# Kernel optimization log

Hardware: AMD Instinct MI355X
Metric: run time of the kernel (lower is better)

## Reference

```python
import jax, jax.numpy as jnp
import numpy as np
import math

CHUNK = 256
NUM_HEADS = 4
EPS = 1e-5


def setup_inputs() -> dict:
    key = jax.random.key(0)
    ks = jax.random.split(key, 12)
    B, N, F = 4, 2048, 256
    x = jax.random.normal(ks[0], (B, N, F), dtype=jnp.float32)
    adj_matrix = jax.random.randint(ks[1], (N, N), 0, 2, dtype=jnp.int32)
    s = 1.0 / math.sqrt(F)
    Wq = jax.random.normal(ks[2], (F, F), dtype=jnp.float32) * s
    bq = jnp.zeros((F,), dtype=jnp.float32)
    Wk = jax.random.normal(ks[3], (F, F), dtype=jnp.float32) * s
    bk = jnp.zeros((F,), dtype=jnp.float32)
    Wv = jax.random.normal(ks[4], (F, F), dtype=jnp.float32) * s
    bv = jnp.zeros((F,), dtype=jnp.float32)
    Wo = jax.random.normal(ks[5], (F, F), dtype=jnp.float32) * s
    bo = jnp.zeros((F,), dtype=jnp.float32)
    gamma = jnp.ones((F,), dtype=jnp.float32)
    beta = jnp.zeros((F,), dtype=jnp.float32)
    return {"x": x, "adj_matrix": adj_matrix, "Wq": Wq, "bq": bq, "Wk": Wk,
            "bk": bk, "Wv": Wv, "bv": bv, "Wo": Wo, "bo": bo,
            "gamma": gamma, "beta": beta}


def reference(x, adj_matrix, Wq, bq, Wk, bk, Wv, bv, Wo, bo, gamma, beta):
    B, N, Fin = x.shape
    H = NUM_HEADS
    Dout = Wq.shape[0]
    Dh = Dout // H
    Nc = N // CHUNK  # number of key chunks

    # projections -> [B, H, N, Dh]
    q = (x @ Wq.T + bq).reshape(B, N, H, Dh).transpose(0, 2, 1, 3)
    k = (x @ Wk.T + bk).reshape(B, N, H, Dh).transpose(0, 2, 1, 3)
    v = (x @ Wv.T + bv).reshape(B, N, H, Dh).transpose(0, 2, 1, 3)

    # key/value chunks: [B, H, Nc, CHUNK, Dh]
    kc = k.reshape(B, H, Nc, CHUNK, Dh)
    vc = v.reshape(B, H, Nc, CHUNK, Dh)

    # scores per key chunk: [B, H, N, Nc, CHUNK]
    scores = jnp.einsum('bhnd,bhjcd->bhnjc', q, kc) / jnp.sqrt(
        jnp.asarray(Dh, dtype=q.dtype))
    scores = jnp.clip(scores, -10.0, 10.0)
    # adjacency mask, chunked along keys: [1, 1, N, Nc, CHUNK]
    mask = adj_matrix.reshape(N, Nc, CHUNK)[None, None]
    scores = jnp.where(mask == 0, jnp.asarray(-10.0, scores.dtype), scores)

    # FAITHFUL quirk: softmax is taken per key chunk (last axis only) and the
    # per-chunk contexts are SUMMED -> total attention mass per query is Nc.
    attn = jax.nn.softmax(scores, axis=-1)
    ctx = jnp.einsum('bhnjc,bhjcd->bhnd', attn, vc)  # sum over chunks j

    ctx = ctx.transpose(0, 2, 1, 3).reshape(B, N, Dout)
    out = ctx @ Wo.T + bo
    out = out + x  # residual (in_features == out_features)

    mu = jnp.mean(out, axis=-1, keepdims=True)
    var = jnp.mean(jnp.square(out - mu), axis=-1, keepdims=True)
    out = (out - mu) * jax.lax.rsqrt(var + EPS) * gamma + beta
    return out
```

## Files before the change

kernel.cpp:

```cpp
#include <hip/hip_runtime.h>
#include <math.h>

#define B_     4
#define N_     2048
#define F_     256
#define H_     4
#define DH     64
#define BN     8192
#define SP     72
#define SPW    264

#define QSCALE 0.18033688011112042f
#define CLIP   14.426950408889634f

typedef _Float16 f16;
typedef _Float16 half8  __attribute__((ext_vector_type(8)));
typedef _Float16 half4v __attribute__((ext_vector_type(4)));
typedef float    floatx4 __attribute__((ext_vector_type(4)));
typedef unsigned long long u64;

__device__ __forceinline__ half8 cvt8(float4 a, float4 b) {
    half8 h;
    h[0] = (f16)a.x; h[1] = (f16)a.y; h[2] = (f16)a.z; h[3] = (f16)a.w;
    h[4] = (f16)b.x; h[5] = (f16)b.y; h[6] = (f16)b.z; h[7] = (f16)b.w;
    return h;
}

__global__ __launch_bounds__(256) void pack_adj(
    const int* __restrict__ adj, u64* __restrict__ P)
{
    const int row   = blockIdx.x >> 3;
    const int chunk = blockIdx.x & 7;
    const int wave  = threadIdx.x >> 6, lane = threadIdx.x & 63;
    const int key   = chunk * 256 + wave * 64 + lane;
    u64 m = __ballot(adj[(size_t)row * N_ + key] != 0);
    if (lane == 0) P[(size_t)row * 32 + chunk * 4 + wave] = m;
}

__global__ __launch_bounds__(256) void cvt_wo(
    const float* __restrict__ Wo, f16* __restrict__ Woh)
{
    const int idx = (blockIdx.x * 256 + threadIdx.x) * 4;
    float4 v = *(const float4*)(Wo + idx);
    half4v h; h[0] = (f16)v.x; h[1] = (f16)v.y; h[2] = (f16)v.z; h[3] = (f16)v.w;
    *(half4v*)(Woh + idx) = h;
}

__global__ __launch_bounds__(256) void proj_mfma(
    const float* __restrict__ x,
    const float* __restrict__ Wq, const float* __restrict__ Wk, const float* __restrict__ Wv,
    const float* __restrict__ bq, const float* __restrict__ bk, const float* __restrict__ bv,
    f16* __restrict__ Qh, f16* __restrict__ Kh, f16* __restrict__ Vt)
{
    const int which = blockIdx.z;
    const float* W    = which == 0 ? Wq : which == 1 ? Wk : Wv;
    const float* bias = which == 0 ? bq : which == 1 ? bk : bv;

    const int r0 = blockIdx.x * 64;
    const int hy = blockIdx.y;
    const int c0 = hy * 64;
    const int tid  = threadIdx.x;
    const int wave = tid >> 6, lane = tid & 63;
    const int quad = lane >> 4, l16 = lane & 15;
    const int row = tid >> 2, seg = tid & 3;

    __shared__ f16 xs[64 * SP];
    __shared__ f16 wsm[64 * SP];

    floatx4 zz = {0.f, 0.f, 0.f, 0.f};
    floatx4 acc[4] = {zz, zz, zz, zz};

    for (int f0 = 0; f0 < F_; f0 += 64) {
        const float* xsrc = x + (size_t)(r0 + row) * F_ + f0 + seg * 16;
        const float* wsrc = W + (size_t)(c0 + row) * F_ + f0 + seg * 16;
        float4 xa0 = *(const float4*)(xsrc + 0), xa1 = *(const float4*)(xsrc + 4);
        float4 xa2 = *(const float4*)(xsrc + 8), xa3 = *(const float4*)(xsrc + 12);
        float4 wa0 = *(const float4*)(wsrc + 0), wa1 = *(const float4*)(wsrc + 4);
        float4 wa2 = *(const float4*)(wsrc + 8), wa3 = *(const float4*)(wsrc + 12);
        __syncthreads();
        *(half8*)&xs[row * SP + seg * 16]      = cvt8(xa0, xa1);
        *(half8*)&xs[row * SP + seg * 16 + 8]  = cvt8(xa2, xa3);
        *(half8*)&wsm[row * SP + seg * 16]     = cvt8(wa0, wa1);
        *(half8*)&wsm[row * SP + seg * 16 + 8] = cvt8(wa2, wa3);
        __syncthreads();
#pragma unroll
        for (int s = 0; s < 2; s++) {
            half8 af = *(const half8*)&xs[(wave * 16 + l16) * SP + s * 32 + quad * 8];
#pragma unroll
            for (int ot = 0; ot < 4; ot++) {
                half8 bf = *(const half8*)&wsm[(ot * 16 + l16) * SP + s * 32 + quad * 8];
                acc[ot] = __builtin_amdgcn_mfma_f32_16x16x32_f16(af, bf, acc[ot], 0, 0, 0);
            }
        }
    }

    const int bb = r0 >> 11, nn0 = r0 & (N_ - 1);

    if (which == 2) {
#pragma unroll
        for (int ot = 0; ot < 4; ot++) {
            const float bv_ = bias[c0 + ot * 16 + l16];
            half4v h4;
#pragma unroll
            for (int r = 0; r < 4; r++) h4[r] = (f16)(acc[ot][r] + bv_);
            *(half4v*)(Vt + (((size_t)bb * H_ + hy) * DH + ot * 16 + l16) * N_
                          + nn0 + wave * 16 + quad * 4) = h4;
        }
    } else {
        const float scl = (which == 0) ? QSCALE : 1.0f;
        f16* dst = which == 0 ? Qh : Kh;
        __syncthreads();
        f16* outb = xs;
#pragma unroll
        for (int ot = 0; ot < 4; ot++) {
            const float bv_ = bias[c0 + ot * 16 + l16];
#pragma unroll
            for (int r = 0; r < 4; r++)
                outb[(wave * 16 + quad * 4 + r) * SP + ot * 16 + l16] =
                    (f16)((acc[ot][r] + bv_) * scl);
        }
        __syncthreads();
        f16* g = dst + (((size_t)bb * H_ + hy) * N_ + nn0 + row) * DH + seg * 16;
        *(float4*)(g)     = *(const float4*)&outb[row * SP + seg * 16];
        *(float4*)(g + 8) = *(const float4*)&outb[row * SP + seg * 16 + 8];
    }
}

__global__ __launch_bounds__(256) void attn_mfma(
    const f16* __restrict__ Qh, const f16* __restrict__ Kh,
    const f16* __restrict__ Vt, const u64* __restrict__ Padj,
    f16* __restrict__ CTXP)
{
    const int nt = blockIdx.x & 31;
    const int sp = blockIdx.x >> 5;
    const int qb = nt * 64;
    const int h  = blockIdx.y;
    const int b  = blockIdx.z;
    const int bh = b * H_ + h;
    const int tid  = threadIdx.x;
    const int wave = tid >> 6, lane = tid & 63;
    const int quad = lane >> 4, l16 = lane & 15;
    const int row = tid >> 2, seg = tid & 3;

    __shared__ f16 QPs[64 * SP];
    __shared__ f16 Ks[64 * SP];
    __shared__ f16 Vs[64 * SP];

    {
        const f16* src = Qh + ((size_t)bh * N_ + qb + row) * DH + seg * 16;
        *(float4*)&QPs[row * SP + seg * 16]     = *(const float4*)(src);
        *(float4*)&QPs[row * SP + seg * 16 + 8] = *(const float4*)(src + 8);
    }
    __syncthreads();
    const half8 qf0 = *(const half8*)&QPs[(wave * 16 + l16) * SP + quad * 8];
    const half8 qf1 = *(const half8*)&QPs[(wave * 16 + l16) * SP + 32 + quad * 8];
    f16* Ps = QPs + wave * 16 * SP;

    const int qglob = qb + wave * 16 + l16;
    const u64* arow = Padj + (size_t)qglob * 32;

    floatx4 zz = {0.f, 0.f, 0.f, 0.f};
    floatx4 ctx_tot[4] = {zz, zz, zz, zz};

    for (int ci = 0; ci < 2; ci++) {
        const int c = sp * 2 + ci;
        floatx4 ctx_ch[4] = {zz, zz, zz, zz};
        float rs_ch = 0.f;

        for (int kt = 0; kt < 4; kt++) {
            const int k0 = c * 256 + kt * 64;
            const f16* ksrc = Kh + ((size_t)bh * N_ + k0 + row) * DH + seg * 16;
            const f16* vsrc = Vt + ((size_t)bh * DH + row) * N_ + k0 + seg * 16;
            float4 ka0 = *(const float4*)(ksrc), ka1 = *(const float4*)(ksrc + 8);
            float4 va0 = *(const float4*)(vsrc), va1 = *(const float4*)(vsrc + 8);
            __syncthreads();
            *(float4*)&Ks[row * SP + seg * 16]     = ka0;
            *(float4*)&Ks[row * SP + seg * 16 + 8] = ka1;
            *(float4*)&Vs[row * SP + seg * 16]     = va0;
            *(float4*)&Vs[row * SP + seg * 16 + 8] = va1;
            __syncthreads();

            const u64 aw = arow[k0 >> 6];
            float rs = 0.f;
#pragma unroll
            for (int m = 0; m < 4; m++) {
                floatx4 sacc = zz;
                half8 a0 = *(const half8*)&Ks[(m * 16 + l16) * SP + quad * 8];
                half8 a1 = *(const half8*)&Ks[(m * 16 + l16) * SP + 32 + quad * 8];
                sacc = __builtin_amdgcn_mfma_f32_16x16x32_f16(a0, qf0, sacc, 0, 0, 0);
                sacc = __builtin_amdgcn_mfma_f32_16x16x32_f16(a1, qf1, sacc, 0, 0, 0);
                const unsigned int nib = (unsigned int)(aw >> (m * 16 + quad * 4)) & 0xFu;
                half4v pv;
#pragma unroll
                for (int r = 0; r < 4; r++) {
                    float sv = fminf(fmaxf(sacc[r], -CLIP), CLIP);
                    sv = ((nib >> r) & 1u) ? sv : -CLIP;
                    const float ev = __builtin_amdgcn_exp2f(sv);
                    rs += ev;
                    pv[r] = (f16)ev;
                }
                *(half4v*)&Ps[l16 * SP + m * 16 + quad * 4] = pv;
            }
            rs += __shfl_xor(rs, 16);
            rs += __shfl_xor(rs, 32);
            rs_ch += rs;

            const half8 p0 = *(const half8*)&Ps[l16 * SP + quad * 8];
            const half8 p1 = *(const half8*)&Ps[l16 * SP + 32 + quad * 8];
#pragma unroll
            for (int m = 0; m < 4; m++) {
                half8 va = *(const half8*)&Vs[(m * 16 + l16) * SP + quad * 8];
                half8 vb = *(const half8*)&Vs[(m * 16 + l16) * SP + 32 + quad * 8];
                ctx_ch[m] = __builtin_amdgcn_mfma_f32_16x16x32_f16(va, p0, ctx_ch[m], 0, 0, 0);
                ctx_ch[m] = __builtin_amdgcn_mfma_f32_16x16x32_f16(vb, p1, ctx_ch[m], 0, 0, 0);
            }
        }

        const float inv = 1.0f / rs_ch;
#pragma unroll
        for (int m = 0; m < 4; m++)
#pragma unroll
            for (int r = 0; r < 4; r++)
                ctx_tot[m][r] += ctx_ch[m][r] * inv;
    }

    f16* dst = CTXP + (((size_t)sp * B_ + b) * N_ + qglob) * F_ + h * DH;
#pragma unroll
    for (int m = 0; m < 4; m++) {
        half4v h4;
#pragma unroll
        for (int r = 0; r < 4; r++) h4[r] = (f16)ctx_tot[m][r];
        *(half4v*)&dst[m * 16 + quad * 4] = h4;
    }
}

__global__ __launch_bounds__(256) void out_mfma(
    const f16* __restrict__ CTXP, const float* __restrict__ x,
    const f16* __restrict__ Woh, const float* __restrict__ bo,
    const float* __restrict__ gamma, const float* __restrict__ beta,
    float* __restrict__ out)
{
    const int n0 = blockIdx.x * 16;
    const int tid  = threadIdx.x;
    const int wave = tid >> 6, lane = tid & 63;
    const int quad = lane >> 4, l16 = lane & 15;
    const int wrow = tid >> 2, wseg = tid & 3;

    __shared__ f16 cs[16 * SPW];
    __shared__ f16 wtile[256 * SP];
    __shared__ float red0[4][16], red1[4][16];

    {
        const int row = tid >> 4, c0 = (tid & 15) * 16;
        const size_t S = (size_t)BN * F_;
        const f16* p = CTXP + (size_t)(n0 + row) * F_ + c0;
#pragma unroll
        for (int g = 0; g < 2; g++) {
            half8 s0 = *(const half8*)(p + g * 8);
            half8 s1 = *(const half8*)(p + S + g * 8);
            half8 s2 = *(const half8*)(p + 2 * S + g * 8);
            half8 s3 = *(const half8*)(p + 3 * S + g * 8);
            half8 o;
#pragma unroll
            for (int e = 0; e < 8; e++)
                o[e] = (f16)(((float)s0[e] + (float)s1[e]) + ((float)s2[e] + (float)s3[e]));
            *(half8*)&cs[row * SPW + c0 + g * 8] = o;
        }
    }

    floatx4 zz = {0.f, 0.f, 0.f, 0.f};
    floatx4 acc[4] = {zz, zz, zz, zz};

#pragma unroll
    for (int f0 = 0; f0 < F_; f0 += 64) {
        __syncthreads();
#pragma unroll
        for (int rr = 0; rr < 4; rr++) {
            const int o = rr * 64 + wrow;
            const f16* src = Woh + (size_t)o * F_ + f0 + wseg * 16;
            *(float4*)&wtile[o * SP + wseg * 16]     = *(const float4*)(src);
            *(float4*)&wtile[o * SP + wseg * 16 + 8] = *(const float4*)(src + 8);
        }
        __syncthreads();
        half8 a0 = *(const half8*)&cs[l16 * SPW + f0 + quad * 8];
        half8 a1 = *(const half8*)&cs[l16 * SPW + f0 + 32 + quad * 8];
#pragma unroll
        for (int ot = 0; ot < 4; ot++) {
            const int o = wave * 64 + ot * 16 + l16;
            half8 b0 = *(const half8*)&wtile[o * SP + quad * 8];
            half8 b1 = *(const half8*)&wtile[o * SP + 32 + quad * 8];
            acc[ot] = __builtin_amdgcn_mfma_f32_16x16x32_f16(a0, b0, acc[ot], 0, 0, 0);
            acc[ot] = __builtin_amdgcn_mfma_f32_16x16x32_f16(a1, b1, acc[ot], 0, 0, 0);
        }
    }

#pragma unroll
    for (int ot = 0; ot < 4; ot++) {
        const int o = wave * 64 + ot * 16 + l16;
        const float bo_ = bo[o];
#pragma unroll
        for (int r = 0; r < 4; r++)
            acc[ot][r] += bo_ + x[(size_t)(n0 + quad * 4 + r) * F_ + o];
    }

#pragma unroll
    for (int r = 0; r < 4; r++) {
        float s = (acc[0][r] + acc[1][r]) + (acc[2][r] + acc[3][r]);
        float q = (acc[0][r] * acc[0][r] + acc[1][r] * acc[1][r]) +
                  (acc[2][r] * acc[2][r] + acc[3][r] * acc[3][r]);
        s += __shfl_xor(s, 1); q += __shfl_xor(q, 1);
        s += __shfl_xor(s, 2); q += __shfl_xor(q, 2);
        s += __shfl_xor(s, 4); q += __shfl_xor(q, 4);
        s += __shfl_xor(s, 8); q += __shfl_xor(q, 8);
        if (l16 == 0) { red0[wave][quad * 4 + r] = s; red1[wave][quad * 4 + r] = q; }
    }
    __syncthreads();

#pragma unroll
    for (int r = 0; r < 4; r++) {
        const int rr = quad * 4 + r;
        const float S  = (red0[0][rr] + red0[1][rr]) + (red0[2][rr] + red0[3][rr]);
        const float Q2 = (red1[0][rr] + red1[1][rr]) + (red1[2][rr] + red1[3][rr]);
        const float mu  = S * (1.0f / F_);
        const float var = Q2 * (1.0f / F_) - mu * mu;
        const float inv = rsqrtf(var + 1e-5f);
#pragma unroll
        for (int ot = 0; ot < 4; ot++) {
            const int o = wave * 64 + ot * 16 + l16;
            out[(size_t)(n0 + rr) * F_ + o] =
                (acc[ot][r] - mu) * inv * gamma[o] + beta[o];
        }
    }
}

extern "C" void kernel_launch(void* const* d_in, const int* in_sizes, int n_in,
                              void* d_out, int out_size, void* d_ws, size_t ws_size,
                              hipStream_t stream)
{
    const float* x     = (const float*)d_in[0];
    const int*   adj   = (const int*)  d_in[1];
    const float* Wq    = (const float*)d_in[2];
    const float* bq    = (const float*)d_in[3];
    const float* Wk    = (const float*)d_in[4];
    const float* bk    = (const float*)d_in[5];
    const float* Wv    = (const float*)d_in[6];
    const float* bv    = (const float*)d_in[7];
    const float* Wo    = (const float*)d_in[8];
    const float* bo    = (const float*)d_in[9];
    const float* gamma = (const float*)d_in[10];
    const float* beta  = (const float*)d_in[11];
    float* out = (float*)d_out;

    float* ws = (float*)d_ws;
    f16*   CTXP = (f16*)(ws);
    f16*   Qh   = (f16*)(ws + 4194304);
    f16*   Kh   = (f16*)(ws + 5242880);
    f16*   Vt   = (f16*)(ws + 6291456);
    u64*   Padj = (u64*)(ws + 7340032);
    f16*   Woh  = (f16*)(ws + 7471104);

    hipLaunchKernelGGL(pack_adj, dim3(N_ * 8), dim3(256), 0, stream, adj, Padj);
    hipLaunchKernelGGL(cvt_wo, dim3(64), dim3(256), 0, stream, Wo, Woh);
    hipLaunchKernelGGL(proj_mfma, dim3(BN / 64, H_, 3), dim3(256), 0, stream,
                       x, Wq, Wk, Wv, bq, bk, bv, Qh, Kh, Vt);
    hipLaunchKernelGGL(attn_mfma, dim3(128, H_, B_), dim3(256), 0, stream,
                       Qh, Kh, Vt, Padj, CTXP);
    hipLaunchKernelGGL(out_mfma, dim3(BN / 16), dim3(256), 0, stream,
                       CTXP, x, Woh, bo, gamma, beta, out);
}
```

Before: 159.9 us.

## Merge prep kernels, pre-convert inputs to fp16, widen projection and attention tiles

```diff
diff --git a/kernel.cpp b/kernel.cpp
--- a/kernel.cpp
+++ b/kernel.cpp
@@ -8,6 +8,7 @@
 #define DH     64
 #define BN     8192
 #define SP     72
+#define SPO    136
 #define SPW    264
 
 #define QSCALE 0.18033688011112042f
@@ -19,78 +20,83 @@
 typedef float    floatx4 __attribute__((ext_vector_type(4)));
 typedef unsigned long long u64;
 
-__device__ __forceinline__ half8 cvt8(float4 a, float4 b) {
-    half8 h;
-    h[0] = (f16)a.x; h[1] = (f16)a.y; h[2] = (f16)a.z; h[3] = (f16)a.w;
-    h[4] = (f16)b.x; h[5] = (f16)b.y; h[6] = (f16)b.z; h[7] = (f16)b.w;
-    return h;
-}
-
-__global__ __launch_bounds__(256) void pack_adj(
-    const int* __restrict__ adj, u64* __restrict__ P)
-{
-    const int row   = blockIdx.x >> 3;
-    const int chunk = blockIdx.x & 7;
-    const int wave  = threadIdx.x >> 6, lane = threadIdx.x & 63;
-    const int key   = chunk * 256 + wave * 64 + lane;
-    u64 m = __ballot(adj[(size_t)row * N_ + key] != 0);
-    if (lane == 0) P[(size_t)row * 32 + chunk * 4 + wave] = m;
-}
-
-__global__ __launch_bounds__(256) void cvt_wo(
+__global__ __launch_bounds__(256) void prep_kernel(
+    const int* __restrict__ adj, u64* __restrict__ P,
+    const float* __restrict__ x,  f16* __restrict__ xh,
+    const float* __restrict__ Wq, f16* __restrict__ Wqh,
+    const float* __restrict__ Wk, f16* __restrict__ Wkh,
+    const float* __restrict__ Wv, f16* __restrict__ Wvh,
     const float* __restrict__ Wo, f16* __restrict__ Woh)
 {
-    const int idx = (blockIdx.x * 256 + threadIdx.x) * 4;
-    float4 v = *(const float4*)(Wo + idx);
+    const int bid = blockIdx.x;
+    if (bid < 16384) {
+        const int row   = bid >> 3;
+        const int chunk = bid & 7;
+        const int wave  = threadIdx.x >> 6, lane = threadIdx.x & 63;
+        const int key   = chunk * 256 + wave * 64 + lane;
+        u64 m = __ballot(adj[(size_t)row * N_ + key] != 0);
+        if (lane == 0) P[(size_t)row * 32 + chunk * 4 + wave] = m;
+        return;
+    }
+    const float* src; f16* dst; int base;
+    if      (bid < 16448) { src = Wo; dst = Woh; base = (bid - 16384) * 1024; }
+    else if (bid < 16512) { src = Wq; dst = Wqh; base = (bid - 16448) * 1024; }
+    else if (bid < 16576) { src = Wk; dst = Wkh; base = (bid - 16512) * 1024; }
+    else if (bid < 16640) { src = Wv; dst = Wvh; base = (bid - 16576) * 1024; }
+    else                  { src = x;  dst = xh;  base = (bid - 16640) * 1024; }
+    const int idx = base + threadIdx.x * 4;
+    float4 v = *(const float4*)(src + idx);
     half4v h; h[0] = (f16)v.x; h[1] = (f16)v.y; h[2] = (f16)v.z; h[3] = (f16)v.w;
-    *(half4v*)(Woh + idx) = h;
+    *(half4v*)(dst + idx) = h;
 }
 
 __global__ __launch_bounds__(256) void proj_mfma(
-    const float* __restrict__ x,
-    const float* __restrict__ Wq, const float* __restrict__ Wk, const float* __restrict__ Wv,
+    const f16* __restrict__ xh,
+    const f16* __restrict__ Wqh, const f16* __restrict__ Wkh, const f16* __restrict__ Wvh,
     const float* __restrict__ bq, const float* __restrict__ bk, const float* __restrict__ bv,
     f16* __restrict__ Qh, f16* __restrict__ Kh, f16* __restrict__ Vt)
 {
     const int which = blockIdx.z;
-    const float* W    = which == 0 ? Wq : which == 1 ? Wk : Wv;
-    const float* bias = which == 0 ? bq : which == 1 ? bk : bv;
+    const f16*   W    = which == 0 ? Wqh : which == 1 ? Wkh : Wvh;
+    const float* bias = which == 0 ? bq  : which == 1 ? bk  : bv;
 
     const int r0 = blockIdx.x * 64;
-    const int hy = blockIdx.y;
-    const int c0 = hy * 64;
+    const int c0 = blockIdx.y * 128;
     const int tid  = threadIdx.x;
     const int wave = tid >> 6, lane = tid & 63;
     const int quad = lane >> 4, l16 = lane & 15;
-    const int row = tid >> 2, seg = tid & 3;
-
-    __shared__ f16 xs[64 * SP];
-    __shared__ f16 wsm[64 * SP];
+    const int row  = tid >> 2, seg  = tid & 3;
+    const int wrow = tid >> 1, whalf = (tid & 1) * 32;
+
+    __shared__ f16 smem[(64 + 128) * SP];
+    f16* xs = smem;
+    f16* wt = smem + 64 * SP;
 
     floatx4 zz = {0.f, 0.f, 0.f, 0.f};
-    floatx4 acc[4] = {zz, zz, zz, zz};
+    floatx4 acc[8] = {zz, zz, zz, zz, zz, zz, zz, zz};
 
     for (int f0 = 0; f0 < F_; f0 += 64) {
-        const float* xsrc = x + (size_t)(r0 + row) * F_ + f0 + seg * 16;
-        const float* wsrc = W + (size_t)(c0 + row) * F_ + f0 + seg * 16;
-        float4 xa0 = *(const float4*)(xsrc + 0), xa1 = *(const float4*)(xsrc + 4);
-        float4 xa2 = *(const float4*)(xsrc + 8), xa3 = *(const float4*)(xsrc + 12);
-        float4 wa0 = *(const float4*)(wsrc + 0), wa1 = *(const float4*)(wsrc + 4);
-        float4 wa2 = *(const float4*)(wsrc + 8), wa3 = *(const float4*)(wsrc + 12);
-        __syncthreads();
-        *(half8*)&xs[row * SP + seg * 16]      = cvt8(xa0, xa1);
-        *(half8*)&xs[row * SP + seg * 16 + 8]  = cvt8(xa2, xa3);
-        *(half8*)&wsm[row * SP + seg * 16]     = cvt8(wa0, wa1);
-        *(half8*)&wsm[row * SP + seg * 16 + 8] = cvt8(wa2, wa3);
-        __syncthreads();
-#pragma unroll
-        for (int s = 0; s < 2; s++) {
-            half8 af = *(const half8*)&xs[(wave * 16 + l16) * SP + s * 32 + quad * 8];
-#pragma unroll
-            for (int ot = 0; ot < 4; ot++) {
-                half8 bf = *(const half8*)&wsm[(ot * 16 + l16) * SP + s * 32 + quad * 8];
-                acc[ot] = __builtin_amdgcn_mfma_f32_16x16x32_f16(af, bf, acc[ot], 0, 0, 0);
-            }
+        const f16* xsrc = xh + (size_t)(r0 + row) * F_ + f0 + seg * 16;
+        const f16* wsrc = W  + (size_t)(c0 + wrow) * F_ + f0 + whalf;
+        float4 xa0 = *(const float4*)(xsrc),      xa1 = *(const float4*)(xsrc + 8);
+        float4 wa0 = *(const float4*)(wsrc),      wa1 = *(const float4*)(wsrc + 8);
+        float4 wa2 = *(const float4*)(wsrc + 16), wa3 = *(const float4*)(wsrc + 24);
+        __syncthreads();
+        *(float4*)&xs[row * SP + seg * 16]      = xa0;
+        *(float4*)&xs[row * SP + seg * 16 + 8]  = xa1;
+        *(float4*)&wt[wrow * SP + whalf]        = wa0;
+        *(float4*)&wt[wrow * SP + whalf + 8]    = wa1;
+        *(float4*)&wt[wrow * SP + whalf + 16]   = wa2;
+        *(float4*)&wt[wrow * SP + whalf + 24]   = wa3;
+        __syncthreads();
+        half8 a0 = *(const half8*)&xs[(wave * 16 + l16) * SP + quad * 8];
+        half8 a1 = *(const half8*)&xs[(wave * 16 + l16) * SP + 32 + quad * 8];
+#pragma unroll
+        for (int ot = 0; ot < 8; ot++) {
+            half8 b0 = *(const half8*)&wt[(ot * 16 + l16) * SP + quad * 8];
+            half8 b1 = *(const half8*)&wt[(ot * 16 + l16) * SP + 32 + quad * 8];
+            acc[ot] = __builtin_amdgcn_mfma_f32_16x16x32_f16(a0, b0, acc[ot], 0, 0, 0);
+            acc[ot] = __builtin_amdgcn_mfma_f32_16x16x32_f16(a1, b1, acc[ot], 0, 0, 0);
         }
     }
 
@@ -98,58 +104,64 @@
 
     if (which == 2) {
 #pragma unroll
-        for (int ot = 0; ot < 4; ot++) {
-            const float bv_ = bias[c0 + ot * 16 + l16];
+        for (int ot = 0; ot < 8; ot++) {
+            const int o  = c0 + ot * 16 + l16;
+            const int hy = o >> 6, dh = o & 63;
+            const float bv_ = bias[o];
             half4v h4;
 #pragma unroll
             for (int r = 0; r < 4; r++) h4[r] = (f16)(acc[ot][r] + bv_);
-            *(half4v*)(Vt + (((size_t)bb * H_ + hy) * DH + ot * 16 + l16) * N_
+            *(half4v*)(Vt + (((size_t)bb * H_ + hy) * DH + dh) * N_
                           + nn0 + wave * 16 + quad * 4) = h4;
         }
     } else {
         const float scl = (which == 0) ? QSCALE : 1.0f;
         f16* dst = which == 0 ? Qh : Kh;
         __syncthreads();
-        f16* outb = xs;
-#pragma unroll
-        for (int ot = 0; ot < 4; ot++) {
+        f16* outb = smem;
+#pragma unroll
+        for (int ot = 0; ot < 8; ot++) {
             const float bv_ = bias[c0 + ot * 16 + l16];
 #pragma unroll
             for (int r = 0; r < 4; r++)
-                outb[(wave * 16 + quad * 4 + r) * SP + ot * 16 + l16] =
+                outb[(wave * 16 + quad * 4 + r) * SPO + ot * 16 + l16] =
                     (f16)((acc[ot][r] + bv_) * scl);
         }
         __syncthreads();
-        f16* g = dst + (((size_t)bb * H_ + hy) * N_ + nn0 + row) * DH + seg * 16;
-        *(float4*)(g)     = *(const float4*)&outb[row * SP + seg * 16];
-        *(float4*)(g + 8) = *(const float4*)&outb[row * SP + seg * 16 + 8];
-    }
-}
-
-__global__ __launch_bounds__(256) void attn_mfma(
+        const int colb = seg * 32;
+        const int hh = (c0 + colb) >> 6, dcol = (c0 + colb) & 63;
+        f16* g = dst + (((size_t)bb * H_ + hh) * N_ + nn0 + row) * DH + dcol;
+#pragma unroll
+        for (int k = 0; k < 4; k++)
+            *(float4*)(g + k * 8) = *(const float4*)&outb[row * SPO + colb + k * 8];
+    }
+}
+
+__global__ __launch_bounds__(512) void attn_mfma(
     const f16* __restrict__ Qh, const f16* __restrict__ Kh,
     const f16* __restrict__ Vt, const u64* __restrict__ Padj,
     f16* __restrict__ CTXP)
 {
-    const int nt = blockIdx.x & 31;
-    const int sp = blockIdx.x >> 5;
-    const int qb = nt * 64;
+    const int nt = blockIdx.x & 15;
+    const int sp = blockIdx.x >> 4;
+    const int qb = nt * 128;
     const int h  = blockIdx.y;
     const int b  = blockIdx.z;
     const int bh = b * H_ + h;
     const int tid  = threadIdx.x;
     const int wave = tid >> 6, lane = tid & 63;
     const int quad = lane >> 4, l16 = lane & 15;
-    const int row = tid >> 2, seg = tid & 3;
-
-    __shared__ f16 QPs[64 * SP];
+    const int qrow = tid >> 2, qseg = tid & 3;
+    const int kvr  = tid >> 3, kvs  = tid & 7;
+
+    __shared__ f16 QPs[128 * SP];
     __shared__ f16 Ks[64 * SP];
     __shared__ f16 Vs[64 * SP];
 
     {
-        const f16* src = Qh + ((size_t)bh * N_ + qb + row) * DH + seg * 16;
-        *(float4*)&QPs[row * SP + seg * 16]     = *(const float4*)(src);
-        *(float4*)&QPs[row * SP + seg * 16 + 8] = *(const float4*)(src + 8);
+        const f16* src = Qh + ((size_t)bh * N_ + qb + qrow) * DH + qseg * 16;
+        *(float4*)&QPs[qrow * SP + qseg * 16]     = *(const float4*)(src);
+        *(float4*)&QPs[qrow * SP + qseg * 16 + 8] = *(const float4*)(src + 8);
     }
     __syncthreads();
     const half8 qf0 = *(const half8*)&QPs[(wave * 16 + l16) * SP + quad * 8];
@@ -169,15 +181,13 @@
 
         for (int kt = 0; kt < 4; kt++) {
             const int k0 = c * 256 + kt * 64;
-            const f16* ksrc = Kh + ((size_t)bh * N_ + k0 + row) * DH + seg * 16;
-            const f16* vsrc = Vt + ((size_t)bh * DH + row) * N_ + k0 + seg * 16;
-            float4 ka0 = *(const float4*)(ksrc), ka1 = *(const float4*)(ksrc + 8);
-            float4 va0 = *(const float4*)(vsrc), va1 = *(const float4*)(vsrc + 8);
+            const f16* ksrc = Kh + ((size_t)bh * N_ + k0 + kvr) * DH + kvs * 8;
+            const f16* vsrc = Vt + ((size_t)bh * DH + kvr) * N_ + k0 + kvs * 8;
+            float4 ka = *(const float4*)(ksrc);
+            float4 va = *(const float4*)(vsrc);
             __syncthreads();
-            *(float4*)&Ks[row * SP + seg * 16]     = ka0;
-            *(float4*)&Ks[row * SP + seg * 16 + 8] = ka1;
-            *(float4*)&Vs[row * SP + seg * 16]     = va0;
-            *(float4*)&Vs[row * SP + seg * 16 + 8] = va1;
+            *(float4*)&Ks[kvr * SP + kvs * 8] = ka;
+            *(float4*)&Vs[kvr * SP + kvs * 8] = va;
             __syncthreads();
 
             const u64 aw = arow[k0 >> 6];
@@ -209,10 +219,10 @@
             const half8 p1 = *(const half8*)&Ps[l16 * SP + 32 + quad * 8];
 #pragma unroll
             for (int m = 0; m < 4; m++) {
-                half8 va = *(const half8*)&Vs[(m * 16 + l16) * SP + quad * 8];
-                half8 vb = *(const half8*)&Vs[(m * 16 + l16) * SP + 32 + quad * 8];
-                ctx_ch[m] = __builtin_amdgcn_mfma_f32_16x16x32_f16(va, p0, ctx_ch[m], 0, 0, 0);
-                ctx_ch[m] = __builtin_amdgcn_mfma_f32_16x16x32_f16(vb, p1, ctx_ch[m], 0, 0, 0);
+                half8 va8 = *(const half8*)&Vs[(m * 16 + l16) * SP + quad * 8];
+                half8 vb8 = *(const half8*)&Vs[(m * 16 + l16) * SP + 32 + quad * 8];
+                ctx_ch[m] = __builtin_amdgcn_mfma_f32_16x16x32_f16(va8, p0, ctx_ch[m], 0, 0, 0);
+                ctx_ch[m] = __builtin_amdgcn_mfma_f32_16x16x32_f16(vb8, p1, ctx_ch[m], 0, 0, 0);
             }
         }
 
@@ -358,12 +368,16 @@
     f16*   Vt   = (f16*)(ws + 6291456);
     u64*   Padj = (u64*)(ws + 7340032);
     f16*   Woh  = (f16*)(ws + 7471104);
-
-    hipLaunchKernelGGL(pack_adj, dim3(N_ * 8), dim3(256), 0, stream, adj, Padj);
-    hipLaunchKernelGGL(cvt_wo, dim3(64), dim3(256), 0, stream, Wo, Woh);
-    hipLaunchKernelGGL(proj_mfma, dim3(BN / 64, H_, 3), dim3(256), 0, stream,
-                       x, Wq, Wk, Wv, bq, bk, bv, Qh, Kh, Vt);
-    hipLaunchKernelGGL(attn_mfma, dim3(128, H_, B_), dim3(256), 0, stream,
+    f16*   xh   = CTXP;
+    f16*   Wqh  = (f16*)(ws + 1048576);
+    f16*   Wkh  = (f16*)(ws + 1081344);
+    f16*   Wvh  = (f16*)(ws + 1114112);
+
+    hipLaunchKernelGGL(prep_kernel, dim3(18688), dim3(256), 0, stream,
+                       adj, Padj, x, xh, Wq, Wqh, Wk, Wkh, Wv, Wvh, Wo, Woh);
+    hipLaunchKernelGGL(proj_mfma, dim3(BN / 64, 2, 3), dim3(256), 0, stream,
+                       xh, Wqh, Wkh, Wvh, bq, bk, bv, Qh, Kh, Vt);
+    hipLaunchKernelGGL(attn_mfma, dim3(64, H_, B_), dim3(512), 0, stream,
                        Qh, Kh, Vt, Padj, CTXP);
     hipLaunchKernelGGL(out_mfma, dim3(BN / 16), dim3(256), 0, stream,
                        CTXP, x, Woh, bo, gamma, beta, out);
```

New measurement: 154.6 us. 3.4% less time.
